# Kernel optimization log

Measured on AMD Instinct MI355X. Metric: run time of the kernel, lower is better.

## Reference

```python
import jax, jax.numpy as jnp
import numpy as np

EMBED = 1024
HEADS = 16
HEAD_DIM = EMBED // HEADS


def setup_inputs() -> dict:
    key = jax.random.key(0)
    ks = jax.random.split(key, 11)
    s = 1.0 / np.sqrt(EMBED)
    B, L = 4, 2048
    return {
        "query": jax.random.normal(ks[0], (B, L, EMBED), jnp.float32),
        "key":   jax.random.normal(ks[1], (B, L, EMBED), jnp.float32),
        "value": jax.random.normal(ks[2], (B, L, EMBED), jnp.float32),
        "Wq": jax.random.normal(ks[3], (EMBED, EMBED), jnp.float32) * s,
        "bq": jnp.zeros((EMBED,), jnp.float32),
        "Wk": jax.random.normal(ks[4], (EMBED, EMBED), jnp.float32) * s,
        "bk": jnp.zeros((EMBED,), jnp.float32),
        "Wv": jax.random.normal(ks[5], (EMBED, EMBED), jnp.float32) * s,
        "bv": jnp.zeros((EMBED,), jnp.float32),
        "Wo": jax.random.normal(ks[6], (EMBED, EMBED), jnp.float32) * s,
        "bo": jnp.zeros((EMBED,), jnp.float32),
    }


def reference(query, key, value, Wq, bq, Wk, bk, Wv, bv, Wo, bo):
    N, Lq, E = query.shape
    Lk = key.shape[1]
    # linear projections (torch nn.Linear: x @ W.T + b)
    q = (query @ Wq.T + bq).reshape(N, Lq, HEADS, HEAD_DIM)
    k = (key   @ Wk.T + bk).reshape(N, Lk, HEADS, HEAD_DIM)
    v = (value @ Wv.T + bv).reshape(N, Lk, HEADS, HEAD_DIM)
    # scaled dot-product attention; note: original scales by sqrt(embed_size)
    scale = 1.0 / jnp.sqrt(jnp.float32(E))
    energy = jnp.einsum('nqhd,nkhd->nhqk', q, k) * scale  # [N,H,Lq,Lk]
    score = jax.nn.softmax(energy, axis=-1)
    out = jnp.einsum('nhqk,nkhd->nqhd', score, v).reshape(N, Lq, E)
    return out @ Wo.T + bo
```

## Files before the change

### kernel.cpp

```cpp
#include <hip/hip_runtime.h>
#include <stdint.h>

#define EMBED 1024
#define HEADS 16
#define HDIM 64
#define BATCH 4
#define SEQ 2048
#define ROWS (BATCH*SEQ)
#define QROWS 128

typedef __attribute__((ext_vector_type(8))) __bf16 bf16x8;
typedef __attribute__((ext_vector_type(4))) float f32x4;

#define LDS_U32(p) ((__attribute__((address_space(3))) unsigned int*)(p))
#define GLB_U32(p) ((const __attribute__((address_space(1))) unsigned int*)(p))

__device__ inline unsigned short f2bf(float f) {
    union { float f; unsigned int u; } v; v.f = f;
    unsigned int u = v.u;
    return (unsigned short)((u + 0x7FFFu + ((u >> 16) & 1u)) >> 16);
}

__global__ __launch_bounds__(256) void cvt3(const float* __restrict__ s0, const float* __restrict__ s1,
                                            const float* __restrict__ s2,
                                            unsigned short* __restrict__ d0, unsigned short* __restrict__ d1,
                                            unsigned short* __restrict__ d2) {
    const float* src = (blockIdx.y == 0) ? s0 : (blockIdx.y == 1) ? s1 : s2;
    unsigned short* dst = (blockIdx.y == 0) ? d0 : (blockIdx.y == 1) ? d1 : d2;
    int i = (blockIdx.x * 256 + threadIdx.x) * 4;
    float4 v = *(const float4*)(src + i);
    uint2 p;
    p.x = (unsigned)f2bf(v.x) | ((unsigned)f2bf(v.y) << 16);
    p.y = (unsigned)f2bf(v.z) | ((unsigned)f2bf(v.w) << 16);
    *(uint2*)(dst + i) = p;
}
__global__ __launch_bounds__(256) void cvt4(const float* __restrict__ s0, const float* __restrict__ s1,
                                            const float* __restrict__ s2, const float* __restrict__ s3,
                                            unsigned short* __restrict__ dst, int stride) {
    const float* src = (blockIdx.y == 0) ? s0 : (blockIdx.y == 1) ? s1 : (blockIdx.y == 2) ? s2 : s3;
    unsigned short* d = dst + (size_t)blockIdx.y * stride;
    int i = (blockIdx.x * 256 + threadIdx.x) * 4;
    float4 v = *(const float4*)(src + i);
    uint2 p;
    p.x = (unsigned)f2bf(v.x) | ((unsigned)f2bf(v.y) << 16);
    p.y = (unsigned)f2bf(v.z) | ((unsigned)f2bf(v.w) << 16);
    *(uint2*)(d + i) = p;
}

template <bool OUT_BF16, bool QKV>
__global__ __launch_bounds__(256) void gemm_bt(const unsigned short* __restrict__ A0,
                                               const unsigned short* __restrict__ B0,
                                               const float* __restrict__ bias0,
                                               const float* __restrict__ bias1,
                                               const float* __restrict__ bias2,
                                               void* __restrict__ C0,
                                               float scale0,
                                               int M, int N, int K) {
    __shared__ unsigned short As[128 * 64];
    __shared__ unsigned short Bs[128 * 64];

    const int tid  = threadIdx.x;
    const int lane = tid & 63;
    const int wave = tid >> 6;
    const int l15  = lane & 15;
    const int quad = lane >> 4;
    const int wm   = wave & 1;
    const int wn   = wave >> 1;
    const int tileM = blockIdx.y * 128;
    const int tileN = blockIdx.x * 128;

    const unsigned short* A = A0;
    const unsigned short* B = B0;
    const float* bias = bias0;
    void* C = C0;
    float scale = QKV ? scale0 : 1.0f;
    if (QKV) {
        int z = blockIdx.z;
        A = A0 + (size_t)z * M * K;
        B = B0 + (size_t)z * N * K;
        bias = (z == 0) ? bias0 : (z == 1) ? bias1 : bias2;
        C = (void*)((unsigned short*)C0 + (size_t)z * M * N);
        if (z != 0) scale = 1.0f;
    }

    f32x4 acc[4][4] = {};

    for (int k0 = 0; k0 < K; k0 += 64) {
        __syncthreads();
#pragma unroll
        for (int s = 0; s < 4; ++s) {
            int j = tid + s * 256;
            int r = j >> 3;
            int c8 = (j & 7) ^ (r & 7);
            __builtin_amdgcn_global_load_lds(GLB_U32(A + (size_t)(tileM + r) * K + k0 + c8 * 8),
                                             LDS_U32(As + j * 8), 16, 0, 0);
            __builtin_amdgcn_global_load_lds(GLB_U32(B + (size_t)(tileN + r) * K + k0 + c8 * 8),
                                             LDS_U32(Bs + j * 8), 16, 0, 0);
        }
        __syncthreads();

#pragma unroll
        for (int kc = 0; kc < 2; ++kc) {
            bf16x8 a[4], b[4];
#pragma unroll
            for (int i = 0; i < 4; ++i) {
                int ra = wm * 64 + i * 16 + l15;
                a[i] = *(const bf16x8*)(As + ra * 64 + (((kc * 4 + quad) ^ (ra & 7)) * 8));
                int rb = wn * 64 + i * 16 + l15;
                b[i] = *(const bf16x8*)(Bs + rb * 64 + (((kc * 4 + quad) ^ (rb & 7)) * 8));
            }
#pragma unroll
            for (int i = 0; i < 4; ++i)
#pragma unroll
                for (int jn = 0; jn < 4; ++jn)
                    acc[i][jn] = __builtin_amdgcn_mfma_f32_16x16x32_bf16(a[i], b[jn], acc[i][jn], 0, 0, 0);
        }
    }

#pragma unroll
    for (int i = 0; i < 4; ++i) {
        int row0 = tileM + wm * 64 + i * 16 + (quad << 2);
#pragma unroll
        for (int jn = 0; jn < 4; ++jn) {
            int col = tileN + wn * 64 + jn * 16 + l15;
            float bv = bias[col];
#pragma unroll
            for (int r = 0; r < 4; ++r) {
                float v = (acc[i][jn][r] + bv) * scale;
                if (OUT_BF16)
                    ((unsigned short*)C)[(size_t)(row0 + r) * N + col] = f2bf(v);
                else
                    ((float*)C)[(size_t)(row0 + r) * N + col] = v;
            }
        }
    }
}

__global__ __launch_bounds__(256) void transpose_v(const unsigned short* __restrict__ src,
                                                   unsigned short* __restrict__ dst) {
    __shared__ unsigned short T[64 * 65];
    const int tid = threadIdx.x;
    const int st = blockIdx.x;
    const int h  = blockIdx.y;
    const int b  = blockIdx.z;

#pragma unroll
    for (int s = 0; s < 2; ++s) {
        int j = tid + s * 256;
        int r = j >> 3;
        int c = (j & 7) * 8;
        unsigned short tmp[8];
        *(uint4*)tmp = *(const uint4*)(src + ((size_t)b * SEQ + st * 64 + r) * EMBED + h * HDIM + c);
#pragma unroll
        for (int i = 0; i < 8; ++i)
            T[r * 65 + c + i] = tmp[i];
    }
    __syncthreads();
#pragma unroll
    for (int s = 0; s < 2; ++s) {
        int j = tid + s * 256;
        int d  = j >> 3;
        int c8 = (j & 7) * 8;
        unsigned short tmp[8];
#pragma unroll
        for (int i = 0; i < 8; ++i)
            tmp[i] = T[(c8 + i) * 65 + d];
        *(uint4*)(dst + ((size_t)(b * HEADS + h) * HDIM + d) * SEQ + st * 64 + c8) = *(uint4*)tmp;
    }
}

__global__ __launch_bounds__(256, 4) void attn(const unsigned short* __restrict__ Q,
                                               const unsigned short* __restrict__ Kp,
                                               const unsigned short* __restrict__ Vt,
                                               unsigned short* __restrict__ O) {
    __shared__ unsigned short KVs[2][2][64 * 64];

    const int tid  = threadIdx.x;
    const int lane = tid & 63;
    const int wave = tid >> 6;
    const int l15  = lane & 15;
    const int quad = lane >> 4;
    const int qt = blockIdx.x;
    const int h  = blockIdx.y;
    const int b  = blockIdx.z;

    const size_t rowbase = (size_t)b * SEQ;
    const int colbase = h * HDIM;
    const size_t vtbase = (size_t)(b * HEADS + h) * HDIM;

#pragma unroll
    for (int s = 0; s < 2; ++s) {
        int j = tid + s * 256;
        int r = j >> 3;
        int sr = (r & 35) | ((r & 12) << 1) | ((r & 16) >> 2);
        int c8 = (j & 7) ^ (r & 7);
        __builtin_amdgcn_global_load_lds(GLB_U32(Kp + (rowbase + sr) * EMBED + colbase + c8 * 8),
                                         LDS_U32(KVs[0][0] + j * 8), 16, 0, 0);
        __builtin_amdgcn_global_load_lds(GLB_U32(Vt + (vtbase + r) * SEQ + c8 * 8),
                                         LDS_U32(KVs[0][1] + j * 8), 16, 0, 0);
    }

    bf16x8 aq[2][2];
#pragma unroll
    for (int mf = 0; mf < 2; ++mf) {
        const unsigned short* qp =
            Q + (rowbase + qt * QROWS + wave * 32 + mf * 16 + l15) * EMBED + colbase;
#pragma unroll
        for (int ks = 0; ks < 2; ++ks)
            aq[mf][ks] = *(const bf16x8*)(qp + ks * 32 + quad * 8);
    }

    f32x4 oacc[2][4] = {};
    float lsum[2] = {};

    for (int t = 0; t < 32; ++t) {
        __syncthreads();
        if (t + 1 < 32) {
            int nb = (t + 1) & 1;
#pragma unroll
            for (int s = 0; s < 2; ++s) {
                int j = tid + s * 256;
                int r = j >> 3;
                int sr = (r & 35) | ((r & 12) << 1) | ((r & 16) >> 2);
                int c8 = (j & 7) ^ (r & 7);
                __builtin_amdgcn_global_load_lds(GLB_U32(Kp + (rowbase + (t + 1) * 64 + sr) * EMBED + colbase + c8 * 8),
                                                 LDS_U32(KVs[nb][0] + j * 8), 16, 0, 0);
                __builtin_amdgcn_global_load_lds(GLB_U32(Vt + (vtbase + r) * SEQ + (t + 1) * 64 + c8 * 8),
                                                 LDS_U32(KVs[nb][1] + j * 8), 16, 0, 0);
            }
        }
        const unsigned short* Ks = KVs[t & 1][0];
        const unsigned short* Vs = KVs[t & 1][1];

        f32x4 sacc[2][4] = {};
#pragma unroll
        for (int ks = 0; ks < 2; ++ks)
#pragma unroll
            for (int nf = 0; nf < 4; ++nf) {
                int krow = nf * 16 + l15;
                int ch = (ks * 4 + quad) ^ (krow & 7);
                bf16x8 bk = *(const bf16x8*)(Ks + krow * 64 + ch * 8);
#pragma unroll
                for (int mf = 0; mf < 2; ++mf)
                    sacc[mf][nf] = __builtin_amdgcn_mfma_f32_16x16x32_bf16(bk, aq[mf][ks], sacc[mf][nf], 0, 0, 0);
            }

        bf16x8 apv[2][2];
#pragma unroll
        for (int mf = 0; mf < 2; ++mf)
#pragma unroll
            for (int nf = 0; nf < 4; ++nf) {
                int ks2 = nf >> 1;
                int jb = (nf & 1) * 4;
                __bf16 h0 = (__bf16)__builtin_amdgcn_exp2f(sacc[mf][nf][0]);
                __bf16 h1 = (__bf16)__builtin_amdgcn_exp2f(sacc[mf][nf][1]);
                __bf16 h2 = (__bf16)__builtin_amdgcn_exp2f(sacc[mf][nf][2]);
                __bf16 h3 = (__bf16)__builtin_amdgcn_exp2f(sacc[mf][nf][3]);
                lsum[mf] += ((float)h0 + (float)h1) + ((float)h2 + (float)h3);
                apv[mf][ks2][jb + 0] = h0;
                apv[mf][ks2][jb + 1] = h1;
                apv[mf][ks2][jb + 2] = h2;
                apv[mf][ks2][jb + 3] = h3;
            }

#pragma unroll
        for (int ks = 0; ks < 2; ++ks) {
#pragma unroll
            for (int df = 0; df < 4; ++df) {
                int vrow = df * 16 + l15;
                int ch = (ks * 4 + quad) ^ (vrow & 7);
                bf16x8 bv = *(const bf16x8*)(Vs + vrow * 64 + ch * 8);
                oacc[0][df] = __builtin_amdgcn_mfma_f32_16x16x32_bf16(apv[0][ks], bv, oacc[0][df], 0, 0, 0);
                oacc[1][df] = __builtin_amdgcn_mfma_f32_16x16x32_bf16(apv[1][ks], bv, oacc[1][df], 0, 0, 0);
            }
        }
    }

    float rinv[2][4];
#pragma unroll
    for (int mf = 0; mf < 2; ++mf) {
        float s = lsum[mf];
        s += __shfl_xor(s, 16);
        s += __shfl_xor(s, 32);
        float ri = 1.0f / s;
#pragma unroll
        for (int r = 0; r < 4; ++r)
            rinv[mf][r] = __shfl(ri, quad * 4 + r);
    }

#pragma unroll
    for (int mf = 0; mf < 2; ++mf)
#pragma unroll
        for (int df = 0; df < 4; ++df) {
            int col = colbase + df * 16 + l15;
#pragma unroll
            for (int r = 0; r < 4; ++r) {
                int row = qt * QROWS + wave * 32 + mf * 16 + quad * 4 + r;
                O[(rowbase + row) * EMBED + col] = f2bf(oacc[mf][df][r] * rinv[mf][r]);
            }
        }
}

extern "C" void kernel_launch(void* const* d_in, const int* in_sizes, int n_in,
                              void* d_out, int out_size, void* d_ws, size_t ws_size,
                              hipStream_t stream) {
    const float* q_in = (const float*)d_in[0];
    const float* k_in = (const float*)d_in[1];
    const float* v_in = (const float*)d_in[2];
    const float* Wq = (const float*)d_in[3];
    const float* bq = (const float*)d_in[4];
    const float* Wk = (const float*)d_in[5];
    const float* bk = (const float*)d_in[6];
    const float* Wv = (const float*)d_in[7];
    const float* bv = (const float*)d_in[8];
    const float* Wo = (const float*)d_in[9];
    const float* bo = (const float*)d_in[10];
    float* out = (float*)d_out;

    const size_t XE = (size_t)ROWS * EMBED;
    const size_t WE = (size_t)EMBED * EMBED;

    unsigned short* ws = (unsigned short*)d_ws;
    unsigned short* xq = ws;
    unsigned short* xk = xq + XE;
    unsigned short* xv = xk + XE;
    unsigned short* wqkvo = xv + XE;
    unsigned short* wo = wqkvo + 3 * WE;
    unsigned short* Qp = wo + WE;
    unsigned short* Kp = Qp + XE;
    unsigned short* Vp = Kp + XE;
    unsigned short* Ap = Vp + XE;

    const float cexp = 0.045084436f;

    cvt3<<<dim3((unsigned)(XE / 1024), 3), 256, 0, stream>>>(q_in, k_in, v_in, xq, xk, xv);
    cvt4<<<dim3((unsigned)(WE / 1024), 4), 256, 0, stream>>>(Wq, Wk, Wv, Wo, wqkvo, (int)WE);

    gemm_bt<true, true><<<dim3(EMBED / 128, ROWS / 128, 3), 256, 0, stream>>>(
        xq, wqkvo, bq, bk, bv, Qp, cexp, ROWS, EMBED, EMBED);

    transpose_v<<<dim3(SEQ / 64, HEADS, BATCH), 256, 0, stream>>>(Vp, xv);

    attn<<<dim3(SEQ / QROWS, HEADS, BATCH), 256, 0, stream>>>(Qp, Kp, xv, Ap);

    gemm_bt<false, false><<<dim3(EMBED / 128, ROWS / 128), 256, 0, stream>>>(
        Ap, wo, bo, nullptr, nullptr, out, 1.0f, ROWS, EMBED, EMBED);
}
```

Measured before the change: 350.6 us.

## Swizzle workgroup order, compute softmax row sums via MFMA, add setprio

Remaps linear block indices in both the GEMM and attention kernels so consecutive workgroups are spread across XCDs, aiming to improve L2 locality. In attention, the per-element VALU row-sum accumulation and final cross-lane shuffles are replaced by an extra MFMA against a ones vector, which yields row sums directly in the accumulator layout. The QK loop is split so the first k-step starts from a zero accumulator, and s_setprio raises wave priority around the MFMA regions. This adds two MFMAs per tile to remove VALU adds and shuffles, and the swizzle mapping assumes the grid size is divisible by eight.

```diff
diff --git a/kernel.cpp b/kernel.cpp
--- a/kernel.cpp
+++ b/kernel.cpp
@@ -66,8 +66,18 @@
     const int quad = lane >> 4;
     const int wm   = wave & 1;
     const int wn   = wave >> 1;
-    const int tileM = blockIdx.y * 128;
-    const int tileN = blockIdx.x * 128;
+
+    const unsigned nx = gridDim.x, ny = gridDim.y;
+    const unsigned nwg = nx * ny * gridDim.z;
+    const unsigned lin = (blockIdx.z * ny + blockIdx.y) * nx + blockIdx.x;
+    const unsigned swz = (lin & 7) * (nwg >> 3) + (lin >> 3);
+    const unsigned bx = swz % nx;
+    const unsigned rem = swz / nx;
+    const unsigned by = rem % ny;
+    const unsigned bz = rem / ny;
+
+    const int tileM = by * 128;
+    const int tileN = bx * 128;
 
     const unsigned short* A = A0;
     const unsigned short* B = B0;
@@ -75,7 +85,7 @@
     void* C = C0;
     float scale = QKV ? scale0 : 1.0f;
     if (QKV) {
-        int z = blockIdx.z;
+        int z = bz;
         A = A0 + (size_t)z * M * K;
         B = B0 + (size_t)z * N * K;
         bias = (z == 0) ? bias0 : (z == 1) ? bias1 : bias2;
@@ -180,9 +190,12 @@
     const int wave = tid >> 6;
     const int l15  = lane & 15;
     const int quad = lane >> 4;
-    const int qt = blockIdx.x;
-    const int h  = blockIdx.y;
-    const int b  = blockIdx.z;
+
+    const int lin = ((blockIdx.z * HEADS + blockIdx.y) << 4) | blockIdx.x;
+    const int swz = ((lin & 7) << 7) | (lin >> 3);
+    const int qt = swz & 15;
+    const int h  = (swz >> 4) & 15;
+    const int b  = swz >> 8;
 
     const size_t rowbase = (size_t)b * SEQ;
     const int colbase = h * HDIM;
@@ -210,8 +223,13 @@
             aq[mf][ks] = *(const bf16x8*)(qp + ks * 32 + quad * 8);
     }
 
+    const f32x4 fz = {0.0f, 0.0f, 0.0f, 0.0f};
+    bf16x8 vone;
+#pragma unroll
+    for (int i = 0; i < 8; ++i) vone[i] = (__bf16)1.0f;
+
     f32x4 oacc[2][4] = {};
-    float lsum[2] = {};
+    f32x4 sumacc[2] = {};
 
     for (int t = 0; t < 32; ++t) {
         __syncthreads();
@@ -232,18 +250,25 @@
         const unsigned short* Ks = KVs[t & 1][0];
         const unsigned short* Vs = KVs[t & 1][1];
 
-        f32x4 sacc[2][4] = {};
-#pragma unroll
-        for (int ks = 0; ks < 2; ++ks)
-#pragma unroll
-            for (int nf = 0; nf < 4; ++nf) {
-                int krow = nf * 16 + l15;
-                int ch = (ks * 4 + quad) ^ (krow & 7);
-                bf16x8 bk = *(const bf16x8*)(Ks + krow * 64 + ch * 8);
-#pragma unroll
-                for (int mf = 0; mf < 2; ++mf)
-                    sacc[mf][nf] = __builtin_amdgcn_mfma_f32_16x16x32_bf16(bk, aq[mf][ks], sacc[mf][nf], 0, 0, 0);
-            }
+        f32x4 sacc[2][4];
+        __builtin_amdgcn_s_setprio(1);
+#pragma unroll
+        for (int nf = 0; nf < 4; ++nf) {
+            int krow = nf * 16 + l15;
+            int ch = quad ^ (krow & 7);
+            bf16x8 bk = *(const bf16x8*)(Ks + krow * 64 + ch * 8);
+            sacc[0][nf] = __builtin_amdgcn_mfma_f32_16x16x32_bf16(bk, aq[0][0], fz, 0, 0, 0);
+            sacc[1][nf] = __builtin_amdgcn_mfma_f32_16x16x32_bf16(bk, aq[1][0], fz, 0, 0, 0);
+        }
+#pragma unroll
+        for (int nf = 0; nf < 4; ++nf) {
+            int krow = nf * 16 + l15;
+            int ch = (4 + quad) ^ (krow & 7);
+            bf16x8 bk = *(const bf16x8*)(Ks + krow * 64 + ch * 8);
+            sacc[0][nf] = __builtin_amdgcn_mfma_f32_16x16x32_bf16(bk, aq[0][1], sacc[0][nf], 0, 0, 0);
+            sacc[1][nf] = __builtin_amdgcn_mfma_f32_16x16x32_bf16(bk, aq[1][1], sacc[1][nf], 0, 0, 0);
+        }
+        __builtin_amdgcn_s_setprio(0);
 
         bf16x8 apv[2][2];
 #pragma unroll
@@ -252,19 +277,17 @@
             for (int nf = 0; nf < 4; ++nf) {
                 int ks2 = nf >> 1;
                 int jb = (nf & 1) * 4;
-                __bf16 h0 = (__bf16)__builtin_amdgcn_exp2f(sacc[mf][nf][0]);
-                __bf16 h1 = (__bf16)__builtin_amdgcn_exp2f(sacc[mf][nf][1]);
-                __bf16 h2 = (__bf16)__builtin_amdgcn_exp2f(sacc[mf][nf][2]);
-                __bf16 h3 = (__bf16)__builtin_amdgcn_exp2f(sacc[mf][nf][3]);
-                lsum[mf] += ((float)h0 + (float)h1) + ((float)h2 + (float)h3);
-                apv[mf][ks2][jb + 0] = h0;
-                apv[mf][ks2][jb + 1] = h1;
-                apv[mf][ks2][jb + 2] = h2;
-                apv[mf][ks2][jb + 3] = h3;
-            }
-
+                apv[mf][ks2][jb + 0] = (__bf16)__builtin_amdgcn_exp2f(sacc[mf][nf][0]);
+                apv[mf][ks2][jb + 1] = (__bf16)__builtin_amdgcn_exp2f(sacc[mf][nf][1]);
+                apv[mf][ks2][jb + 2] = (__bf16)__builtin_amdgcn_exp2f(sacc[mf][nf][2]);
+                apv[mf][ks2][jb + 3] = (__bf16)__builtin_amdgcn_exp2f(sacc[mf][nf][3]);
+            }
+
+        __builtin_amdgcn_s_setprio(1);
 #pragma unroll
         for (int ks = 0; ks < 2; ++ks) {
+            sumacc[0] = __builtin_amdgcn_mfma_f32_16x16x32_bf16(apv[0][ks], vone, sumacc[0], 0, 0, 0);
+            sumacc[1] = __builtin_amdgcn_mfma_f32_16x16x32_bf16(apv[1][ks], vone, sumacc[1], 0, 0, 0);
 #pragma unroll
             for (int df = 0; df < 4; ++df) {
                 int vrow = df * 16 + l15;
@@ -274,19 +297,15 @@
                 oacc[1][df] = __builtin_amdgcn_mfma_f32_16x16x32_bf16(apv[1][ks], bv, oacc[1][df], 0, 0, 0);
             }
         }
+        __builtin_amdgcn_s_setprio(0);
     }
 
     float rinv[2][4];
 #pragma unroll
-    for (int mf = 0; mf < 2; ++mf) {
-        float s = lsum[mf];
-        s += __shfl_xor(s, 16);
-        s += __shfl_xor(s, 32);
-        float ri = 1.0f / s;
+    for (int mf = 0; mf < 2; ++mf)
 #pragma unroll
         for (int r = 0; r < 4; ++r)
-            rinv[mf][r] = __shfl(ri, quad * 4 + r);
-    }
+            rinv[mf][r] = 1.0f / sumacc[mf][r];
 
 #pragma unroll
     for (int mf = 0; mf < 2; ++mf)
```

After: 326.4 us. 6.9% less time.
